# Optimization experiments

Measured on AMD Instinct MI355X. Metric: run time of the kernel, lower is better.

Reference implementation:

```python
import jax, jax.numpy as jnp
import numpy as np

EPS_R = 1e-6


def setup_inputs() -> dict:
    key = jax.random.key(0)
    k1, k2, k3 = jax.random.split(key, 3)
    N, F, C = 32768, 2048, 64
    X = jax.random.normal(k1, (N, F), dtype=jnp.float32)
    W = jax.random.normal(k2, (C, F), dtype=jnp.float32) * 0.1  # matches init std=0.1
    r = jax.random.uniform(k3, (F,), dtype=jnp.float32)
    return {"X": X, "W": W, "r": r}


def reference(X, W, r):
    # Weighted squared distances: d[n, c] = sum_f r_f * (X[n,f] - W[c,f])**2
    # Expanded form avoids the [N, C, F] intermediate:
    #   d = (X^2) @ r + (W^2) @ r - 2 * X @ (r * W)^T
    rc = jnp.clip(r, EPS_R, None)
    x_sq = (X * X) @ rc                      # [N]
    w_sq = (W * W) @ rc                      # [C]
    cross = X @ (W * rc).T                   # [N, C]  (dominant GEMM)
    dists = x_sq[:, None] + w_sq[None, :] - 2.0 * cross  # [N, C]
    # One prototype per class with label = class index, per init_prototypes.
    preds = jnp.argmin(dists, axis=1)        # [N] int
    return dists, preds
```

## Files before the change

kernel.cpp:

```cpp
#include <hip/hip_runtime.h>

#define NROWS 32768
#define FDIM  2048
#define CDIM  64
#define BM    64
#define BK    32
#define SA    40

#define EPS_R  1e-6f
#define XSCALE 256.0f
#define WSCALE 1024.0f
#define DESCALE (2.0f / (XSCALE * WSCALE))

typedef __attribute__((ext_vector_type(8))) _Float16 half8;
typedef __attribute__((ext_vector_type(4))) float    f32x4;

__device__ __forceinline__ unsigned packh(_Float16 a, _Float16 b) {
    return (unsigned)__builtin_bit_cast(unsigned short, a) |
           ((unsigned)__builtin_bit_cast(unsigned short, b) << 16);
}

__device__ __forceinline__ void split2(float a, float b, unsigned& hi, unsigned& lo) {
    _Float16 ha = (_Float16)a, hb = (_Float16)b;
    _Float16 la = (_Float16)(a - (float)ha), lb = (_Float16)(b - (float)hb);
    hi = packh(ha, hb);
    lo = packh(la, lb);
}

__global__ __launch_bounds__(256) void gmlvq_prep(
    const float* __restrict__ W, const float* __restrict__ r,
    unsigned short* __restrict__ Bh, unsigned short* __restrict__ Bl,
    float* __restrict__ wsq) {
    const int c = blockIdx.x;
    const int tid = threadIdx.x;
    const int f0 = tid * 8;

    const float* Wp = W + (size_t)c * FDIM + f0;
    float4 w0 = *(const float4*)Wp;
    float4 w1 = *(const float4*)(Wp + 4);
    float4 r0 = *(const float4*)(r + f0);
    float4 r1 = *(const float4*)(r + f0 + 4);
    r0.x = fmaxf(r0.x, EPS_R); r0.y = fmaxf(r0.y, EPS_R);
    r0.z = fmaxf(r0.z, EPS_R); r0.w = fmaxf(r0.w, EPS_R);
    r1.x = fmaxf(r1.x, EPS_R); r1.y = fmaxf(r1.y, EPS_R);
    r1.z = fmaxf(r1.z, EPS_R); r1.w = fmaxf(r1.w, EPS_R);

    float rw0 = r0.x * w0.x, rw1 = r0.y * w0.y, rw2 = r0.z * w0.z, rw3 = r0.w * w0.w;
    float rw4 = r1.x * w1.x, rw5 = r1.y * w1.y, rw6 = r1.z * w1.z, rw7 = r1.w * w1.w;

    float part = rw0 * w0.x + rw1 * w0.y + rw2 * w0.z + rw3 * w0.w
               + rw4 * w1.x + rw5 * w1.y + rw6 * w1.z + rw7 * w1.w;

    unsigned h01, l01, h23, l23, h45, l45, h67, l67;
    split2(rw0 * WSCALE, rw1 * WSCALE, h01, l01);
    split2(rw2 * WSCALE, rw3 * WSCALE, h23, l23);
    split2(rw4 * WSCALE, rw5 * WSCALE, h45, l45);
    split2(rw6 * WSCALE, rw7 * WSCALE, h67, l67);

    *(uint4*)(Bh + (size_t)c * FDIM + f0) = make_uint4(h01, h23, h45, h67);
    *(uint4*)(Bl + (size_t)c * FDIM + f0) = make_uint4(l01, l23, l45, l67);

#pragma unroll
    for (int m = 32; m; m >>= 1) part += __shfl_xor(part, m);
    __shared__ float red[4];
    if ((tid & 63) == 0) red[tid >> 6] = part;
    __syncthreads();
    if (tid == 0) wsq[c] = (red[0] + red[1]) + (red[2] + red[3]);
}

__global__ __launch_bounds__(256, 2) void gmlvq_main(
    const float* __restrict__ X, const float* __restrict__ r,
    const unsigned short* __restrict__ Bh, const unsigned short* __restrict__ Bl,
    const float* __restrict__ wsq_g,
    float* __restrict__ dists, float* __restrict__ preds) {

    __shared__ unsigned short lds_ah[BM * SA], lds_al[BM * SA];
    __shared__ unsigned short lds_bh[CDIM * SA], lds_bl[CDIM * SA];
    __shared__ float lds_xsqp[BM][8];
    __shared__ float lds_xsq[BM];
    __shared__ float lds_wsq[CDIM];

    const int tid = threadIdx.x;
    const int row_base = blockIdx.x * BM;

    const int rsub = tid >> 3;
    const int k4   = tid & 7;
    const int kofs = k4 * 4;
    const int cB   = tid >> 2;
    const int segB = (tid & 3) * 8;
    const int wave = tid >> 6;
    const int lane = tid & 63;
    const int quad = lane >> 4;
    const int l15  = lane & 15;

    if (tid < CDIM) lds_wsq[tid] = wsq_g[tid];

    float p0 = 0.f, p1 = 0.f;
    f32x4 acc[4];
#pragma unroll
    for (int n = 0; n < 4; n++) acc[n] = (f32x4){0.f, 0.f, 0.f, 0.f};

    const float* Xp0 = X + (size_t)(row_base + rsub) * FDIM;
    const float* Xp1 = Xp0 + (size_t)32 * FDIM;
    const unsigned short* Bhp = Bh + (size_t)cB * FDIM + segB;
    const unsigned short* Blp = Bl + (size_t)cB * FDIM + segB;

    for (int kk = 0; kk < FDIM; kk += BK) {
        float4 rv = *(const float4*)(r + kk + kofs);
        rv.x = fmaxf(rv.x, EPS_R); rv.y = fmaxf(rv.y, EPS_R);
        rv.z = fmaxf(rv.z, EPS_R); rv.w = fmaxf(rv.w, EPS_R);
        const float4 xv0 = *(const float4*)(Xp0 + kk + kofs);
        const float4 xv1 = *(const float4*)(Xp1 + kk + kofs);
        const uint4 bhv = *(const uint4*)(Bhp + kk);
        const uint4 blv = *(const uint4*)(Blp + kk);

        p0 += rv.x * xv0.x * xv0.x + rv.y * xv0.y * xv0.y
            + rv.z * xv0.z * xv0.z + rv.w * xv0.w * xv0.w;
        p1 += rv.x * xv1.x * xv1.x + rv.y * xv1.y * xv1.y
            + rv.z * xv1.z * xv1.z + rv.w * xv1.w * xv1.w;

        unsigned h0, l0, h1, l1;
        split2(xv0.x * XSCALE, xv0.y * XSCALE, h0, l0);
        split2(xv0.z * XSCALE, xv0.w * XSCALE, h1, l1);
        *(uint2*)&lds_ah[rsub * SA + kofs] = make_uint2(h0, h1);
        *(uint2*)&lds_al[rsub * SA + kofs] = make_uint2(l0, l1);
        split2(xv1.x * XSCALE, xv1.y * XSCALE, h0, l0);
        split2(xv1.z * XSCALE, xv1.w * XSCALE, h1, l1);
        *(uint2*)&lds_ah[(rsub + 32) * SA + kofs] = make_uint2(h0, h1);
        *(uint2*)&lds_al[(rsub + 32) * SA + kofs] = make_uint2(l0, l1);

        *(uint4*)&lds_bh[cB * SA + segB] = bhv;
        *(uint4*)&lds_bl[cB * SA + segB] = blv;

        __syncthreads();

        const half8 ah = *(const half8*)&lds_ah[(wave * 16 + l15) * SA + quad * 8];
        const half8 al = *(const half8*)&lds_al[(wave * 16 + l15) * SA + quad * 8];
#pragma unroll
        for (int n = 0; n < 4; n++) {
            const half8 bhf = *(const half8*)&lds_bh[(n * 16 + l15) * SA + quad * 8];
            const half8 blf = *(const half8*)&lds_bl[(n * 16 + l15) * SA + quad * 8];
            acc[n] = __builtin_amdgcn_mfma_f32_16x16x32_f16(ah, bhf, acc[n], 0, 0, 0);
            acc[n] = __builtin_amdgcn_mfma_f32_16x16x32_f16(ah, blf, acc[n], 0, 0, 0);
            acc[n] = __builtin_amdgcn_mfma_f32_16x16x32_f16(al, bhf, acc[n], 0, 0, 0);
        }
        __syncthreads();
    }

    lds_xsqp[rsub][k4]      = p0;
    lds_xsqp[rsub + 32][k4] = p1;
    __syncthreads();
    if (tid < BM) {
        float sx = 0.f;
#pragma unroll
        for (int j = 0; j < 8; j++) sx += lds_xsqp[tid][j];
        lds_xsq[tid] = sx;
    }
    __syncthreads();

    float dd[4][4];
#pragma unroll
    for (int n = 0; n < 4; n++) {
#pragma unroll
        for (int rr = 0; rr < 4; rr++) {
            const int m = wave * 16 + quad * 4 + rr;
            const int c = n * 16 + l15;
            const float d = lds_xsq[m] + lds_wsq[c] - acc[n][rr] * DESCALE;
            dd[n][rr] = d;
            dists[(size_t)(row_base + m) * CDIM + c] = d;
        }
    }

#pragma unroll
    for (int rr = 0; rr < 4; rr++) {
        float bv = dd[0][rr];
        int   bi = l15;
#pragma unroll
        for (int n = 1; n < 4; n++) {
            const float v = dd[n][rr];
            const int  ci = n * 16 + l15;
            if (v < bv || (v == bv && ci < bi)) { bv = v; bi = ci; }
        }
#pragma unroll
        for (int mask = 1; mask < 16; mask <<= 1) {
            const float ov = __shfl_xor(bv, mask);
            const int   oi = __shfl_xor(bi, mask);
            if (ov < bv || (ov == bv && oi < bi)) { bv = ov; bi = oi; }
        }
        if (l15 == 0) {
            const int m = wave * 16 + quad * 4 + rr;
            preds[row_base + m] = (float)bi;
        }
    }
}

extern "C" void kernel_launch(void* const* d_in, const int* in_sizes, int n_in,
                              void* d_out, int out_size, void* d_ws, size_t ws_size,
                              hipStream_t stream) {
    const float* X = (const float*)d_in[0];
    const float* W = (const float*)d_in[1];
    const float* r = (const float*)d_in[2];
    float* dists = (float*)d_out;
    float* preds = dists + (size_t)NROWS * CDIM;

    unsigned short* Bh = (unsigned short*)d_ws;
    unsigned short* Bl = Bh + (size_t)CDIM * FDIM;
    float* wsq = (float*)(Bl + (size_t)CDIM * FDIM);

    gmlvq_prep<<<dim3(CDIM), dim3(256), 0, stream>>>(W, r, Bh, Bl, wsq);
    gmlvq_main<<<dim3(NROWS / BM), dim3(256), 0, stream>>>(X, r, Bh, Bl, wsq, dists, preds);
}
```

Baseline: 391.3 us.

## Load X fragments directly into MFMA registers and double-buffer prototype tiles

After: 389.2 us. Within noise of the previous version (-0.6%).

```diff
diff --git a/kernel.cpp b/kernel.cpp
--- a/kernel.cpp
+++ b/kernel.cpp
@@ -5,12 +5,11 @@
 #define CDIM  64
 #define BM    64
 #define BK    32
+#define NCH   (FDIM / BK)
 #define SA    40
-
-#define EPS_R  1e-6f
-#define XSCALE 256.0f
+#define EPS_R 1e-6f
 #define WSCALE 1024.0f
-#define DESCALE (2.0f / (XSCALE * WSCALE))
+#define DESCALE (2.0f / WSCALE)
 
 typedef __attribute__((ext_vector_type(8))) _Float16 half8;
 typedef __attribute__((ext_vector_type(4))) float    f32x4;
@@ -30,7 +29,7 @@
 __global__ __launch_bounds__(256) void gmlvq_prep(
     const float* __restrict__ W, const float* __restrict__ r,
     unsigned short* __restrict__ Bh, unsigned short* __restrict__ Bl,
-    float* __restrict__ wsq) {
+    float* __restrict__ wsq, float* __restrict__ rc_out) {
     const int c = blockIdx.x;
     const int tid = threadIdx.x;
     const int f0 = tid * 8;
@@ -45,6 +44,11 @@
     r1.x = fmaxf(r1.x, EPS_R); r1.y = fmaxf(r1.y, EPS_R);
     r1.z = fmaxf(r1.z, EPS_R); r1.w = fmaxf(r1.w, EPS_R);
 
+    if (c == 0) {
+        *(float4*)(rc_out + f0) = r0;
+        *(float4*)(rc_out + f0 + 4) = r1;
+    }
+
     float rw0 = r0.x * w0.x, rw1 = r0.y * w0.y, rw2 = r0.z * w0.z, rw3 = r0.w * w0.w;
     float rw4 = r1.x * w1.x, rw5 = r1.y * w1.y, rw6 = r1.z * w1.z, rw7 = r1.w * w1.w;
 
@@ -68,94 +72,97 @@
     if (tid == 0) wsq[c] = (red[0] + red[1]) + (red[2] + red[3]);
 }
 
-__global__ __launch_bounds__(256, 2) void gmlvq_main(
-    const float* __restrict__ X, const float* __restrict__ r,
+__global__ __launch_bounds__(256, 3) void gmlvq_main(
+    const float* __restrict__ X, const float* __restrict__ rc,
     const unsigned short* __restrict__ Bh, const unsigned short* __restrict__ Bl,
     const float* __restrict__ wsq_g,
     float* __restrict__ dists, float* __restrict__ preds) {
 
-    __shared__ unsigned short lds_ah[BM * SA], lds_al[BM * SA];
-    __shared__ unsigned short lds_bh[CDIM * SA], lds_bl[CDIM * SA];
-    __shared__ float lds_xsqp[BM][8];
+    __shared__ __align__(16) unsigned short lds_bh[2][CDIM * SA];
+    __shared__ __align__(16) unsigned short lds_bl[2][CDIM * SA];
     __shared__ float lds_xsq[BM];
     __shared__ float lds_wsq[CDIM];
 
-    const int tid = threadIdx.x;
-    const int row_base = blockIdx.x * BM;
-
-    const int rsub = tid >> 3;
-    const int k4   = tid & 7;
-    const int kofs = k4 * 4;
-    const int cB   = tid >> 2;
-    const int segB = (tid & 3) * 8;
+    const int tid  = threadIdx.x;
     const int wave = tid >> 6;
     const int lane = tid & 63;
     const int quad = lane >> 4;
     const int l15  = lane & 15;
+    const int row_base = blockIdx.x * BM;
+    const int cB   = tid >> 2;
+    const int segB = (tid & 3) * 8;
 
     if (tid < CDIM) lds_wsq[tid] = wsq_g[tid];
 
-    float p0 = 0.f, p1 = 0.f;
-    f32x4 acc[4];
-#pragma unroll
-    for (int n = 0; n < 4; n++) acc[n] = (f32x4){0.f, 0.f, 0.f, 0.f};
-
-    const float* Xp0 = X + (size_t)(row_base + rsub) * FDIM;
-    const float* Xp1 = Xp0 + (size_t)32 * FDIM;
+    const float* Ap = X + (size_t)(row_base + wave * 16 + l15) * FDIM + quad * 8;
+    const float* Rp = rc + quad * 8;
     const unsigned short* Bhp = Bh + (size_t)cB * FDIM + segB;
     const unsigned short* Blp = Bl + (size_t)cB * FDIM + segB;
 
-    for (int kk = 0; kk < FDIM; kk += BK) {
-        float4 rv = *(const float4*)(r + kk + kofs);
-        rv.x = fmaxf(rv.x, EPS_R); rv.y = fmaxf(rv.y, EPS_R);
-        rv.z = fmaxf(rv.z, EPS_R); rv.w = fmaxf(rv.w, EPS_R);
-        const float4 xv0 = *(const float4*)(Xp0 + kk + kofs);
-        const float4 xv1 = *(const float4*)(Xp1 + kk + kofs);
-        const uint4 bhv = *(const uint4*)(Bhp + kk);
-        const uint4 blv = *(const uint4*)(Blp + kk);
-
-        p0 += rv.x * xv0.x * xv0.x + rv.y * xv0.y * xv0.y
-            + rv.z * xv0.z * xv0.z + rv.w * xv0.w * xv0.w;
-        p1 += rv.x * xv1.x * xv1.x + rv.y * xv1.y * xv1.y
-            + rv.z * xv1.z * xv1.z + rv.w * xv1.w * xv1.w;
-
-        unsigned h0, l0, h1, l1;
-        split2(xv0.x * XSCALE, xv0.y * XSCALE, h0, l0);
-        split2(xv0.z * XSCALE, xv0.w * XSCALE, h1, l1);
-        *(uint2*)&lds_ah[rsub * SA + kofs] = make_uint2(h0, h1);
-        *(uint2*)&lds_al[rsub * SA + kofs] = make_uint2(l0, l1);
-        split2(xv1.x * XSCALE, xv1.y * XSCALE, h0, l0);
-        split2(xv1.z * XSCALE, xv1.w * XSCALE, h1, l1);
-        *(uint2*)&lds_ah[(rsub + 32) * SA + kofs] = make_uint2(h0, h1);
-        *(uint2*)&lds_al[(rsub + 32) * SA + kofs] = make_uint2(l0, l1);
-
-        *(uint4*)&lds_bh[cB * SA + segB] = bhv;
-        *(uint4*)&lds_bl[cB * SA + segB] = blv;
-
+    uint4 b0h = *(const uint4*)(Bhp);
+    uint4 b0l = *(const uint4*)(Blp);
+    *(uint4*)&lds_bh[0][cB * SA + segB] = b0h;
+    *(uint4*)&lds_bl[0][cB * SA + segB] = b0l;
+    uint4 bnh = *(const uint4*)(Bhp + BK);
+    uint4 bnl = *(const uint4*)(Blp + BK);
+
+    float4 a0 = *(const float4*)(Ap);
+    float4 a1 = *(const float4*)(Ap + 4);
+    float4 r0 = *(const float4*)(Rp);
+    float4 r1 = *(const float4*)(Rp + 4);
+
+    float p = 0.f;
+    f32x4 acc[4];
+#pragma unroll
+    for (int n = 0; n < 4; n++) acc[n] = (f32x4){0.f, 0.f, 0.f, 0.f};
+
+#pragma unroll 2
+    for (int c = 0; c < NCH; c++) {
         __syncthreads();
 
-        const half8 ah = *(const half8*)&lds_ah[(wave * 16 + l15) * SA + quad * 8];
-        const half8 al = *(const half8*)&lds_al[(wave * 16 + l15) * SA + quad * 8];
+        const int kn = ((c + 1) & (NCH - 1)) * BK;
+        const int kf = ((c + 2) & (NCH - 1)) * BK;
+        const float4 a0n = *(const float4*)(Ap + kn);
+        const float4 a1n = *(const float4*)(Ap + kn + 4);
+        const float4 r0n = *(const float4*)(Rp + kn);
+        const float4 r1n = *(const float4*)(Rp + kn + 4);
+        const uint4  bfh = *(const uint4*)(Bhp + kf);
+        const uint4  bfl = *(const uint4*)(Blp + kf);
+
+        half8 ah, al;
+        {
+            const float va[8] = {a0.x, a0.y, a0.z, a0.w, a1.x, a1.y, a1.z, a1.w};
+            const float vr[8] = {r0.x, r0.y, r0.z, r0.w, r1.x, r1.y, r1.z, r1.w};
+#pragma unroll
+            for (int j = 0; j < 8; j++) {
+                const float v = va[j];
+                const _Float16 h = (_Float16)v;
+                ah[j] = h;
+                al[j] = (_Float16)(v - (float)h);
+                p += vr[j] * v * v;
+            }
+        }
+
+        const int bb = c & 1;
 #pragma unroll
         for (int n = 0; n < 4; n++) {
-            const half8 bhf = *(const half8*)&lds_bh[(n * 16 + l15) * SA + quad * 8];
-            const half8 blf = *(const half8*)&lds_bl[(n * 16 + l15) * SA + quad * 8];
+            const half8 bhf = *(const half8*)&lds_bh[bb][(n * 16 + l15) * SA + quad * 8];
+            const half8 blf = *(const half8*)&lds_bl[bb][(n * 16 + l15) * SA + quad * 8];
             acc[n] = __builtin_amdgcn_mfma_f32_16x16x32_f16(ah, bhf, acc[n], 0, 0, 0);
             acc[n] = __builtin_amdgcn_mfma_f32_16x16x32_f16(ah, blf, acc[n], 0, 0, 0);
             acc[n] = __builtin_amdgcn_mfma_f32_16x16x32_f16(al, bhf, acc[n], 0, 0, 0);
         }
-        __syncthreads();
-    }
-
-    lds_xsqp[rsub][k4]      = p0;
-    lds_xsqp[rsub + 32][k4] = p1;
-    __syncthreads();
-    if (tid < BM) {
-        float sx = 0.f;
-#pragma unroll
-        for (int j = 0; j < 8; j++) sx += lds_xsqp[tid][j];
-        lds_xsq[tid] = sx;
-    }
+
+        *(uint4*)&lds_bh[bb ^ 1][cB * SA + segB] = bnh;
+        *(uint4*)&lds_bl[bb ^ 1][cB * SA + segB] = bnl;
+
+        bnh = bfh; bnl = bfl;
+        a0 = a0n; a1 = a1n; r0 = r0n; r1 = r1n;
+    }
+
+    p += __shfl_xor(p, 16);
+    p += __shfl_xor(p, 32);
+    if (quad == 0) lds_xsq[wave * 16 + l15] = p;
     __syncthreads();
 
     float dd[4][4];
@@ -164,10 +171,10 @@
 #pragma unroll
         for (int rr = 0; rr < 4; rr++) {
             const int m = wave * 16 + quad * 4 + rr;
-            const int c = n * 16 + l15;
-            const float d = lds_xsq[m] + lds_wsq[c] - acc[n][rr] * DESCALE;
+            const int cc = n * 16 + l15;
+            const float d = lds_xsq[m] + lds_wsq[cc] - acc[n][rr] * DESCALE;
             dd[n][rr] = d;
-            dists[(size_t)(row_base + m) * CDIM + c] = d;
+            dists[(size_t)(row_base + m) * CDIM + cc] = d;
         }
     }
 
@@ -205,8 +212,9 @@
 
     unsigned short* Bh = (unsigned short*)d_ws;
     unsigned short* Bl = Bh + (size_t)CDIM * FDIM;
-    float* wsq = (float*)(Bl + (size_t)CDIM * FDIM);
-
-    gmlvq_prep<<<dim3(CDIM), dim3(256), 0, stream>>>(W, r, Bh, Bl, wsq);
-    gmlvq_main<<<dim3(NROWS / BM), dim3(256), 0, stream>>>(X, r, Bh, Bl, wsq, dists, preds);
-}
+    float* wsq   = (float*)(Bl + (size_t)CDIM * FDIM);
+    float* rc_ws = wsq + CDIM;
+
+    gmlvq_prep<<<dim3(CDIM), dim3(256), 0, stream>>>(W, r, Bh, Bl, wsq, rc_ws);
+    gmlvq_main<<<dim3(NROWS / BM), dim3(256), 0, stream>>>(X, rc_ws, Bh, Bl, wsq, dists, preds);
+}
```
